# Optimization experiments

Hardware: AMD Instinct MI355X
Metric: run time of the kernel (lower is better)

The kernel has to match this reference:

```python
import jax, jax.numpy as jnp
import numpy as np

T = 5
EPS = 1e-05


def setup_inputs() -> dict:
    key = jax.random.key(0)
    X = jax.random.normal(key, (64, 512, 32, 32), dtype=jnp.float32)
    return {"X": X}


def reference(X):
    # IterNorm (training branch): whiten channels via Newton-Schulz inverse sqrt.
    N, C, H, W = X.shape
    x = jnp.transpose(X, (1, 0, 2, 3)).reshape(C, -1)  # [d, m], d=C, m=N*H*W
    d, m = x.shape
    mean = jnp.mean(x, axis=-1, keepdims=True)
    xc = x - mean
    I = jnp.eye(d, dtype=X.dtype)
    # Sigma = eps*I + (1/m) xc xc^T  (addmm(eps, I, 1/m, xc, xc^T))
    Sigma = EPS * I + (xc @ xc.T) / m
    rTr = 1.0 / jnp.trace(Sigma)          # (Sigma * I).sum().reciprocal()
    Sigma_N = Sigma * rTr
    P = I
    for _ in range(T):
        # P_{k+1} = 1.5*P_k - 0.5 * P_k^3 @ Sigma_N
        P = 1.5 * P - 0.5 * (P @ P @ P) @ Sigma_N
    wm = P * jnp.sqrt(rTr)                # whitening matrix ~ Sigma^{-1/2}
    xn = wm @ xc                          # [d, m]
    Xn = jnp.transpose(xn.reshape(C, N, H, W), (1, 0, 2, 3))
    return Xn
```

## Files before the change

### kernel.cpp

```cpp
#include <hip/hip_runtime.h>
#include <math.h>

#define Nn   64
#define Cc   512
#define HWs  1024
#define CHW  (Cc * HWs)
#define Mm   (Nn * HWs)
#define EPSC 1e-5f
#define NBC  128

typedef unsigned int   u32;
typedef unsigned short u16;
typedef unsigned long long u64;
typedef __attribute__((ext_vector_type(8))) short  short8;
typedef __attribute__((ext_vector_type(4))) float  floatx4;

__device__ __forceinline__ u16 f2bf(float f) {
    u32 u = __float_as_uint(f);
    u += 0x7fff + ((u >> 16) & 1);
    return (u16)(u >> 16);
}
__device__ __forceinline__ float bf2f(u16 h) {
    return __uint_as_float(((u32)h) << 16);
}

__device__ __forceinline__ void gld_lds16(const u16* g, u16* l) {
    __builtin_amdgcn_global_load_lds(
        (const __attribute__((address_space(1))) u32*)g,
        (__attribute__((address_space(3))) u32*)l, 16, 0, 0);
}

#define AUX_SC 0x11

__device__ __forceinline__ void gld_lds16_sc(const u16* g, u16* l) {
    __builtin_amdgcn_global_load_lds(
        (const __attribute__((address_space(1))) u32*)g,
        (__attribute__((address_space(3))) u32*)l, 16, 0, AUX_SC);
}
__device__ __forceinline__ void st8_sc(u16* p, u64 pk) {
    asm volatile("global_store_dwordx2 %0, %1, off sc0 sc1"
                 :: "v"(p), "v"(pk) : "memory");
}
__device__ __forceinline__ u64 pk4(const u16* h) {
    return (u64)h[0] | ((u64)h[1] << 16) | ((u64)h[2] << 32) | ((u64)h[3] << 48);
}

__global__ __launch_bounds__(256) void convert_transpose(const float* __restrict__ X,
                                                         u16* __restrict__ Xbf,
                                                         u16* __restrict__ Xt,
                                                         float* __restrict__ meanP) {
    const int hT = blockIdx.x;
    const int h0 = hT << 6;
    const int c0 = blockIdx.y << 6;
    const int n  = blockIdx.z;
    const int t  = threadIdx.x;
    __shared__ u16   T[64][65];
    __shared__ float red[64][17];

    const float* Xn  = X   + (size_t)n * CHW;
    u16*         Xbn = Xbf + (size_t)n * CHW;
    u16*         Xtn = Xt  + (size_t)n * CHW;

    const int cl = t >> 4;
    const int h4 = (t & 15) << 2;
#pragma unroll
    for (int i = 0; i < 4; ++i) {
        const int c = cl + (i << 4);
        float4 v = *(const float4*)&Xn[(size_t)(c0 + c) * HWs + h0 + h4];
        red[c][t & 15] = v.x + v.y + v.z + v.w;
        u16 b0 = f2bf(v.x), b1 = f2bf(v.y), b2 = f2bf(v.z), b3 = f2bf(v.w);
        *(ushort4*)&Xbn[(size_t)(c0 + c) * HWs + h0 + h4] = make_ushort4(b0, b1, b2, b3);
        T[c][h4]     = b0;
        T[c][h4 + 1] = b1;
        T[c][h4 + 2] = b2;
        T[c][h4 + 3] = b3;
    }
    __syncthreads();
    const int hl = t >> 4;
    const int c4 = (t & 15) << 2;
#pragma unroll
    for (int i = 0; i < 4; ++i) {
        const int h = hl + (i << 4);
        ushort4 pk = make_ushort4(T[c4][h], T[c4 + 1][h], T[c4 + 2][h], T[c4 + 3][h]);
        *(ushort4*)&Xtn[(size_t)(h0 + h) * Cc + c0 + c4] = pk;
    }
    if (t < 64) {
        float s = 0.f;
#pragma unroll
        for (int j = 0; j < 16; ++j) s += red[t][j];
        atomicAdd(&meanP[hT * 512 + c0 + t], s);
    }
}

__global__ __launch_bounds__(256) void gram_mfma(const u16* __restrict__ Xbf,
                                                 float* __restrict__ G) {
    static const int TI[10] = {0,0,0,0,1,1,1,2,2,3};
    static const int TJ[10] = {0,1,2,3,1,2,3,2,3,3};
    const int id = blockIdx.x;
    const int q  = id >> 3;
    const int x  = q % 10;
    const int y  = (id & 7) + ((q / 10) << 3);
    const int i0 = TI[x] << 7;
    const int j0 = TJ[x] << 7;
    const int n0 = y << 1;
    const int t  = threadIdx.x;
    const int w  = t >> 6, l = t & 63;

    __shared__ u16 As[2][4096];
    __shared__ u16 Bs[2][4096];

    floatx4 acc[4][4];
#pragma unroll
    for (int mi = 0; mi < 4; ++mi)
#pragma unroll
        for (int ni = 0; ni < 4; ++ni) acc[mi][ni] = (floatx4){0.f, 0.f, 0.f, 0.f};

    const int lr = l >> 2;
    const int lc = (l & 3) << 3;
    const int wm = w >> 1, wn = w & 1;
    const int fm = l & 15, fq = l >> 4;

    auto issue = [&](int s, int bb) {
        const u16* Xn = Xbf + (size_t)(n0 + (s >> 5)) * CHW;
        const int hw  = (s & 31) << 5;
#pragma unroll
        for (int p = 0; p < 2; ++p) {
            const int g   = w * 2 + p;
            const int row = g * 16 + lr;
            gld_lds16(Xn + (size_t)(i0 + row) * HWs + hw + lc, &As[bb][g * 512]);
            gld_lds16(Xn + (size_t)(j0 + row) * HWs + hw + lc, &Bs[bb][g * 512]);
        }
    };

    issue(0, 0);
    __syncthreads();
    for (int s = 0; s < 64; ++s) {
        if (s < 63) issue(s + 1, (s + 1) & 1);
        const int bb = s & 1;
        short8 a[4], b[4];
#pragma unroll
        for (int mi = 0; mi < 4; ++mi)
            a[mi] = *(const short8*)&As[bb][(wm * 64 + mi * 16 + fm) * 32 + fq * 8];
#pragma unroll
        for (int ni = 0; ni < 4; ++ni)
            b[ni] = *(const short8*)&Bs[bb][(wn * 64 + ni * 16 + fm) * 32 + fq * 8];
#pragma unroll
        for (int mi = 0; mi < 4; ++mi)
#pragma unroll
            for (int ni = 0; ni < 4; ++ni)
                acc[mi][ni] = __builtin_amdgcn_mfma_f32_16x16x32_bf16(
                    a[mi], b[ni], acc[mi][ni], 0, 0, 0);
        __syncthreads();
    }
#pragma unroll
    for (int mi = 0; mi < 4; ++mi)
#pragma unroll
        for (int ni = 0; ni < 4; ++ni)
#pragma unroll
            for (int r = 0; r < 4; ++r) {
                const int gi = i0 + wm * 64 + mi * 16 + fq * 4 + r;
                const int gj = j0 + wn * 64 + ni * 16 + fm;
                atomicAdd(&G[(size_t)gi * Cc + gj], acc[mi][ni][r]);
            }
}

__device__ __forceinline__ void gridbar(int* bar, int gen) {
    asm volatile("s_waitcnt vmcnt(0)" ::: "memory");
    __syncthreads();
    if (threadIdx.x == 0) {
        __hip_atomic_fetch_add(bar, 1, __ATOMIC_RELAXED, __HIP_MEMORY_SCOPE_AGENT);
        while (__hip_atomic_load(bar, __ATOMIC_RELAXED, __HIP_MEMORY_SCOPE_AGENT) < gen * NBC)
            __builtin_amdgcn_s_sleep(1);
    }
    __syncthreads();
}

template <int MR>
__device__ __forceinline__ void mm_bk64(const u16* Ah, const u16* Al,
                                        const u16* Bh, const u16* Bl,
                                        int i0, int j0,
                                        float alpha, const float* D, float beta,
                                        float* Cf, u16* Ch, u16* Cl, u16* S) {
    const int t = threadIdx.x, w = t >> 6, l = t & 63;
    const int wm = w >> 1, wn = w & 1, fm = l & 15, fq = l >> 4;
    const int lr = l >> 2, lc = (l & 3) << 3;
    constexpr int MI     = MR / 32;
    constexpr int OFF_AL = MR * 64;
    constexpr int OFF_BH = 2 * MR * 64;
    constexpr int OFF_BL = 2 * MR * 64 + 4096;
    constexpr int BUFSZ  = 2 * MR * 64 + 8192;

    const u16* src  = (w == 0) ? Ah : (w == 1) ? Al : (w == 2) ? Bh : Bl;
    const int rbase = (w < 2) ? i0 : j0;
    const int R     = (w < 2) ? MR : 64;
    const int OFF   = (w == 0) ? 0 : (w == 1) ? OFF_AL : (w == 2) ? OFF_BH : OFF_BL;

    floatx4 acc[MI][2];
#pragma unroll
    for (int mi = 0; mi < MI; ++mi)
#pragma unroll
        for (int ni = 0; ni < 2; ++ni) acc[mi][ni] = (floatx4){0.f, 0.f, 0.f, 0.f};

    auto issue = [&](int c, int bb) {
        u16* dst = S + bb * BUFSZ + OFF;
        const u16* sp = src + (size_t)rbase * 512 + (c << 6);
#pragma unroll
        for (int s = 0; s < 2; ++s)
#pragma unroll 4
            for (int g = 0; g < (R >> 4); ++g)
                gld_lds16_sc(sp + (size_t)(g * 16 + lr) * 512 + s * 32 + lc,
                             dst + s * R * 32 + g * 512);
    };
    auto compute = [&](int bb) {
        const u16* base = S + bb * BUFSZ;
#pragma unroll
        for (int s = 0; s < 2; ++s) {
            short8 ah[MI], al[MI], bh[2], bl[2];
#pragma unroll
            for (int mi = 0; mi < MI; ++mi) {
                const int r = wm * (MR / 2) + mi * 16 + fm;
                const int o = s * MR * 32 + r * 32 + fq * 8;
                ah[mi] = *(const short8*)&base[o];
                al[mi] = *(const short8*)&base[OFF_AL + o];
            }
#pragma unroll
            for (int ni = 0; ni < 2; ++ni) {
                const int r = wn * 32 + ni * 16 + fm;
                const int o = s * 2048 + r * 32 + fq * 8;
                bh[ni] = *(const short8*)&base[OFF_BH + o];
                bl[ni] = *(const short8*)&base[OFF_BL + o];
            }
#pragma unroll
            for (int mi = 0; mi < MI; ++mi)
#pragma unroll
                for (int ni = 0; ni < 2; ++ni) {
                    acc[mi][ni] = __builtin_amdgcn_mfma_f32_16x16x32_bf16(ah[mi], bh[ni], acc[mi][ni], 0, 0, 0);
                    acc[mi][ni] = __builtin_amdgcn_mfma_f32_16x16x32_bf16(ah[mi], bl[ni], acc[mi][ni], 0, 0, 0);
                    acc[mi][ni] = __builtin_amdgcn_mfma_f32_16x16x32_bf16(al[mi], bh[ni], acc[mi][ni], 0, 0, 0);
                }
        }
    };

    issue(0, 0);
    __syncthreads();
    for (int c = 0; c < 8; ++c) {
        if (c < 7) issue(c + 1, (c + 1) & 1);
        compute(c & 1);
        __syncthreads();
    }

#pragma unroll
    for (int mi = 0; mi < MI; ++mi)
#pragma unroll
        for (int ni = 0; ni < 2; ++ni) {
            const int gib = i0 + wm * (MR / 2) + mi * 16 + fq * 4;
            const int gj  = j0 + wn * 32 + ni * 16 + fm;
            u16 h[4], lo[4];
#pragma unroll
            for (int r4 = 0; r4 < 4; ++r4) {
                float v = alpha * acc[mi][ni][r4];
                if (D) v += beta * D[(size_t)(gib + r4) * 512 + gj];
                if (Cf) Cf[(size_t)(gib + r4) * 512 + gj] = v;
                h[r4]  = f2bf(v);
                lo[r4] = f2bf(v - bf2f(h[r4]));
            }
            st8_sc(&Ch[(size_t)gj * 512 + gib], pk4(h));
            st8_sc(&Cl[(size_t)gj * 512 + gib], pk4(lo));
        }
}

__global__ __launch_bounds__(256) void ns_chain(
    const float* G, const float* meanP, float* scal, int* bar, float* wmmv,
    u16* Sh, u16* Sl, u16* PhA, u16* PlA, u16* PhB, u16* PlB,
    u16* T2h, u16* T2l, u16* Wh, u16* Wl, float* PfA, float* PfB) {
    __shared__ u16   S[32768];
    __shared__ float meanL[512];
    __shared__ float redL[4];
    const int t = threadIdx.x, b = blockIdx.x;
    const int w = t >> 6, l = t & 63;

    float tp = 0.f;
#pragma unroll
    for (int cb = 0; cb < 2; ++cb) {
        const int c = t + (cb << 8);
        float s = 0.f;
#pragma unroll
        for (int q = 0; q < 16; ++q) s += meanP[(q << 9) + c];
        const float mc = s * (1.0f / Mm);
        meanL[c] = mc;
        tp += G[(size_t)c * 513] * (1.0f / Mm) - mc * mc;
    }
#pragma unroll
    for (int o = 32; o > 0; o >>= 1) tp += __shfl_xor(tp, o);
    if (l == 0) redL[w] = tp;
    __syncthreads();
    const float tr  = redL[0] + redL[1] + redL[2] + redL[3] + (float)Cc * EPSC;
    const float rtr = 1.0f / tr;
    const float sr  = sqrtf(rtr);
    if (b == 0 && t == 0) { scal[0] = rtr; scal[1] = sr; }

    const int R0 = (b >> 3) << 5;
    const int C0 = (b & 7) << 6;
#pragma unroll
    for (int k2 = 0; k2 < 2; ++k2) {
        const int idx4 = (k2 << 8) + t;
        const int i  = R0 + (idx4 >> 4);
        const int jb = C0 + ((idx4 & 15) << 2);
        float p1[4];
        u16 sh[4], sl[4], ph[4], pl[4];
#pragma unroll
        for (int u = 0; u < 4; ++u) {
            const int j = jb + u;
            const float g = (i <= j) ? G[((size_t)i << 9) + j] : G[((size_t)j << 9) + i];
            float sig = g * (1.0f / Mm) - meanL[i] * meanL[j];
            if (i == j) sig += EPSC;
            const float sN = sig * rtr;
            sh[u] = f2bf(sN);
            sl[u] = f2bf(sN - bf2f(sh[u]));
            p1[u] = ((i == j) ? 1.5f : 0.f) - 0.5f * sN;
            ph[u] = f2bf(p1[u]);
            pl[u] = f2bf(p1[u] - bf2f(ph[u]));
        }
        const size_t e = ((size_t)i << 9) + jb;
        st8_sc(&Sh[e],  pk4(sh));
        st8_sc(&Sl[e],  pk4(sl));
        st8_sc(&PhA[e], pk4(ph));
        st8_sc(&PlA[e], pk4(pl));
        *(float4*)&PfA[e] = make_float4(p1[0], p1[1], p1[2], p1[3]);
    }
    int gen = 0;
    gridbar(bar, ++gen);

    u16 *ph = PhA, *pl = PlA, *qh = PhB, *ql = PlB;
    float *pf = PfA, *qf = PfB;
    const int i0a = ((b & 63) >> 3) << 6, j0a = (b & 7) << 6;
    for (int it = 0; it < 4; ++it) {
        if (b < 64)
            mm_bk64<64>(ph, pl, ph, pl, i0a, j0a, 1.f, nullptr, 0.f,
                        nullptr, T2h, T2l, S);
        else
            mm_bk64<64>(ph, pl, Sh, Sl, i0a, j0a, 1.f, nullptr, 0.f,
                        nullptr, Wh, Wl, S);
        gridbar(bar, ++gen);
        mm_bk64<32>(T2h, T2l, Wh, Wl, R0, C0, -0.5f, pf, 1.5f,
                    qf, qh, ql, S);
        gridbar(bar, ++gen);
        { u16* x = ph; ph = qh; qh = x; }
        { u16* x = pl; pl = ql; ql = x; }
        { float* x = pf; pf = qf; qf = x; }
    }

    {
        const int row = R0 + (t >> 3);
        const int jb  = C0 + ((t & 7) << 3);
        float s = 0.f;
#pragma unroll
        for (int jj = 0; jj < 8; ++jj)
            s += pf[((size_t)row << 9) + jb + jj] * meanL[jb + jj];
        s += __shfl_xor(s, 1);
        s += __shfl_xor(s, 2);
        s += __shfl_xor(s, 4);
        if ((t & 7) == 0) atomicAdd(&wmmv[row], s * sr);
    }
}

__global__ __launch_bounds__(256) void whiten_mfma(const u16* __restrict__ Xt,
                                                   const u16* __restrict__ Pbf,
                                                   const float* __restrict__ wmm,
                                                   const float* __restrict__ scal,
                                                   float* __restrict__ out) {
    const int id  = blockIdx.x;
    const int m   = (id >> 3) & 3;
    const int grp = (id & 7) + ((id >> 5) << 3);
    const int c0  = m << 7;
    const int h0  = (grp & 3) << 8;
    const int n   = grp >> 2;
    const int t   = threadIdx.x;
    const int w   = t >> 6, l = t & 63;

    __shared__ char smem[49152];
    u16* As = (u16*)smem;
    u16* Bs = As + 16384;
    float* Ep = (float*)smem;

    floatx4 acc[8][4];
#pragma unroll
    for (int mi = 0; mi < 8; ++mi)
#pragma unroll
        for (int ni = 0; ni < 4; ++ni) acc[mi][ni] = (floatx4){0.f, 0.f, 0.f, 0.f};

    const int lr = l >> 2;
    const int lc = (l & 3) << 3;
    const int wm = w >> 1, wn = w & 1;
    const int fm = l & 15, fq = l >> 4;

    const u16* Xn = Xt + (size_t)n * CHW;

    auto issue = [&](int k, int bb) {
        const int kk = k << 5;
#pragma unroll
        for (int gi = 0; gi < 4; ++gi) {
            const int g = w * 4 + gi;
            gld_lds16(Xn + (size_t)(h0 + g * 16 + lr) * Cc + kk + lc,
                      &As[bb * 8192 + g * 512]);
        }
#pragma unroll
        for (int p = 0; p < 2; ++p) {
            const int g = w * 2 + p;
            gld_lds16(Pbf + (size_t)(c0 + g * 16 + lr) * Cc + kk + lc,
                      &Bs[bb * 4096 + g * 512]);
        }
    };

    issue(0, 0);
    __syncthreads();
    for (int k = 0; k < 16; ++k) {
        if (k < 15) issue(k + 1, (k + 1) & 1);
        const int bb = k & 1;
        short8 a[8], b[4];
#pragma unroll
        for (int mi = 0; mi < 8; ++mi)
            a[mi] = *(const short8*)&As[bb * 8192 + (wm * 128 + mi * 16 + fm) * 32 + fq * 8];
#pragma unroll
        for (int ni = 0; ni < 4; ++ni)
            b[ni] = *(const short8*)&Bs[bb * 4096 + (wn * 64 + ni * 16 + fm) * 32 + fq * 8];
#pragma unroll
        for (int mi = 0; mi < 8; ++mi)
#pragma unroll
            for (int ni = 0; ni < 4; ++ni)
                acc[mi][ni] = __builtin_amdgcn_mfma_f32_16x16x32_bf16(
                    a[mi], b[ni], acc[mi][ni], 0, 0, 0);
        __syncthreads();
    }

    const float sr = scal[1];
    float wv[4];
#pragma unroll
    for (int ni = 0; ni < 4; ++ni) wv[ni] = wmm[c0 + wn * 64 + ni * 16 + fm];
    float* outn = out + (size_t)n * CHW;

#pragma unroll
    for (int mp = 0; mp < 4; ++mp) {
        __syncthreads();
#pragma unroll
        for (int p = 0; p < 2; ++p) {
            const int mi = mp * 2 + p;
#pragma unroll
            for (int ni = 0; ni < 4; ++ni) {
                const int row  = wn * 64 + ni * 16 + fm;
                const int slot = wm * 32 + p * 16 + fq * 4;
                floatx4 v = acc[mi][ni] * sr - wv[ni];
                *(floatx4*)&Ep[row * 68 + slot] = v;
            }
        }
        __syncthreads();
#pragma unroll
        for (int jj = 0; jj < 8; ++jj) {
            const int idx = jj * 256 + t;
            const int row = idx >> 4;
            const int s4  = (idx & 15) << 2;
            const int wmr = s4 >> 5;
            const int within = s4 & 31;
            float4 v = *(const float4*)&Ep[row * 68 + s4];
            *(float4*)&outn[(size_t)(c0 + row) * HWs + h0 + wmr * 128 + mp * 32 + within] = v;
        }
    }
}

__global__ __launch_bounds__(256) void mean_kernel(const float* __restrict__ X,
                                                   float* __restrict__ mean) {
    const int c = blockIdx.x;
    const int t = threadIdx.x;
    float s = 0.f;
    for (int n = 0; n < Nn; ++n) {
        const float4* p = (const float4*)(X + (size_t)n * CHW + (size_t)c * HWs);
        float4 v = p[t];
        s += v.x + v.y + v.z + v.w;
    }
    __shared__ float red[256];
    red[t] = s;
    __syncthreads();
    for (int o = 128; o > 0; o >>= 1) {
        if (t < o) red[t] += red[t + o];
        __syncthreads();
    }
    if (t == 0) mean[c] = red[0] * (1.0f / Mm);
}

__global__ __launch_bounds__(256) void trace_fb(const float* __restrict__ G,
                                                const float* __restrict__ mean,
                                                float* __restrict__ scal) {
    const int t = threadIdx.x;
    float s = 0.f;
    for (int i = t; i < Cc; i += 256)
        s += G[(size_t)i * Cc + i] * (1.0f / Mm) - mean[i] * mean[i];
    __shared__ float red[256];
    red[t] = s;
    __syncthreads();
    for (int o = 128; o > 0; o >>= 1) {
        if (t < o) red[t] += red[t + o];
        __syncthreads();
    }
    if (t == 0) {
        const float tr  = red[0] + (float)Cc * EPSC;
        const float rtr = 1.0f / tr;
        scal[0] = rtr;
        scal[1] = sqrtf(rtr);
    }
}

__global__ __launch_bounds__(256) void gram_kernel(const float* __restrict__ X,
                                                   float* __restrict__ G) {
    const int ti = blockIdx.x >> 3, tj = blockIdx.x & 7;
    const int i0 = ti << 6, j0 = tj << 6;
    const int n0 = blockIdx.y << 3;
    const int t  = threadIdx.x;
    const int tx = t & 15, ty = t >> 4;
    __shared__ float As[64][33];
    __shared__ float Bs[64][33];
    float acc[4][4] = {};
    const int lc = t & 31;
    const int lr0 = t >> 5;
    for (int n = n0; n < n0 + 8; ++n) {
        const float* Xn = X + (size_t)n * CHW;
        for (int hw0 = 0; hw0 < HWs; hw0 += 32) {
#pragma unroll
            for (int r = 0; r < 8; ++r) {
                const int row = lr0 + (r << 3);
                As[row][lc] = Xn[(size_t)(i0 + row) * HWs + hw0 + lc];
                Bs[row][lc] = Xn[(size_t)(j0 + row) * HWs + hw0 + lc];
            }
            __syncthreads();
#pragma unroll
            for (int k = 0; k < 32; ++k) {
                float a[4], b[4];
#pragma unroll
                for (int r = 0; r < 4; ++r) a[r] = As[(ty << 2) + r][k];
#pragma unroll
                for (int cn = 0; cn < 4; ++cn) b[cn] = Bs[(tx << 2) + cn][k];
#pragma unroll
                for (int r = 0; r < 4; ++r)
#pragma unroll
                    for (int cn = 0; cn < 4; ++cn) acc[r][cn] += a[r] * b[cn];
            }
            __syncthreads();
        }
    }
#pragma unroll
    for (int r = 0; r < 4; ++r)
#pragma unroll
        for (int cn = 0; cn < 4; ++cn)
            atomicAdd(&G[(size_t)(i0 + (ty << 2) + r) * Cc + j0 + (tx << 2) + cn],
                      acc[r][cn]);
}

__global__ __launch_bounds__(256) void sigman_full_kernel(const float* __restrict__ G,
                                                          const float* __restrict__ mean,
                                                          const float* __restrict__ scal,
                                                          float* __restrict__ S,
                                                          float* __restrict__ P) {
    const int e = blockIdx.x * 256 + threadIdx.x;
    const int i = e >> 9, j = e & 511;
    const float rtr = scal[0];
    float sig = G[e] * (1.0f / Mm) - mean[i] * mean[j];
    if (i == j) sig += EPSC;
    S[e] = sig * rtr;
    P[e] = (i == j) ? 1.f : 0.f;
}

__global__ __launch_bounds__(256) void mm512_kernel(const float* __restrict__ A,
                                                    const float* __restrict__ B,
                                                    float* __restrict__ C,
                                                    float alpha,
                                                    const float* __restrict__ D,
                                                    float beta) {
    const int ti = blockIdx.x >> 3, tj = blockIdx.x & 7;
    const int i0 = ti << 6, j0 = tj << 6;
    const int t  = threadIdx.x;
    const int tx = t & 15, ty = t >> 4;
    __shared__ float As[64][33];
    __shared__ float Bs[32][65];
    float acc[4][4] = {};
    const int lcA = t & 31, lrA = t >> 5;
    const int lcB = t & 63, lrB = t >> 6;
    for (int k0 = 0; k0 < 512; k0 += 32) {
#pragma unroll
        for (int r = 0; r < 8; ++r) {
            const int row = lrA + (r << 3);
            As[row][lcA] = A[(size_t)(i0 + row) * 512 + k0 + lcA];
        }
#pragma unroll
        for (int r = 0; r < 8; ++r) {
            const int row = lrB + (r << 2);
            Bs[row][lcB] = B[(size_t)(k0 + row) * 512 + j0 + lcB];
        }
        __syncthreads();
#pragma unroll
        for (int k = 0; k < 32; ++k) {
            float a[4], b[4];
#pragma unroll
            for (int r = 0; r < 4; ++r) a[r] = As[(ty << 2) + r][k];
#pragma unroll
            for (int cn = 0; cn < 4; ++cn) b[cn] = Bs[k][(tx << 2) + cn];
#pragma unroll
            for (int r = 0; r < 4; ++r)
#pragma unroll
                for (int cn = 0; cn < 4; ++cn) acc[r][cn] += a[r] * b[cn];
        }
        __syncthreads();
    }
#pragma unroll
    for (int r = 0; r < 4; ++r) {
        const size_t idx = (size_t)(i0 + (ty << 2) + r) * 512 + j0 + (tx << 2);
        float4 v;
        v.x = alpha * acc[r][0];
        v.y = alpha * acc[r][1];
        v.z = alpha * acc[r][2];
        v.w = alpha * acc[r][3];
        if (D) {
            const float4 d = *(const float4*)(D + idx);
            v.x += beta * d.x; v.y += beta * d.y; v.z += beta * d.z; v.w += beta * d.w;
        }
        *(float4*)(C + idx) = v;
    }
}

__global__ __launch_bounds__(128) void wmm_kernel(const float* __restrict__ P,
                                                  const float* __restrict__ mean,
                                                  const float* __restrict__ scal,
                                                  float* __restrict__ wmm) {
    const int c = blockIdx.x, t = threadIdx.x;
    float s = 0.f;
    for (int j = t; j < Cc; j += 128) s += P[(size_t)c * Cc + j] * mean[j];
    __shared__ float red[128];
    red[t] = s;
    __syncthreads();
    for (int o = 64; o > 0; o >>= 1) {
        if (t < o) red[t] += red[t + o];
        __syncthreads();
    }
    if (t == 0) wmm[c] = red[0] * scal[1];
}

__global__ __launch_bounds__(256) void whiten_kernel(const float* __restrict__ X,
                                                     const float* __restrict__ P,
                                                     const float* __restrict__ wmm,
                                                     const float* __restrict__ scal,
                                                     float* __restrict__ out) {
    const int c0 = blockIdx.x << 6;
    const int h0 = blockIdx.y << 6;
    const int n  = blockIdx.z;
    const int t  = threadIdx.x;
    const int tx = t & 15, ty = t >> 4;
    __shared__ float Ps[64][33];
    __shared__ float Xs[32][65];
    float acc[4][4] = {};
    const int lcA = t & 31, lrA = t >> 5;
    const int lcB = t & 63, lrB = t >> 6;
    const float* Xn = X + (size_t)n * CHW;
    for (int k0 = 0; k0 < 512; k0 += 32) {
#pragma unroll
        for (int r = 0; r < 8; ++r) {
            const int row = lrA + (r << 3);
            Ps[row][lcA] = P[(size_t)(c0 + row) * 512 + k0 + lcA];
        }
#pragma unroll
        for (int r = 0; r < 8; ++r) {
            const int row = lrB + (r << 2);
            Xs[row][lcB] = Xn[(size_t)(k0 + row) * HWs + h0 + lcB];
        }
        __syncthreads();
#pragma unroll
        for (int k = 0; k < 32; ++k) {
            float a[4], b[4];
#pragma unroll
            for (int r = 0; r < 4; ++r) a[r] = Ps[(ty << 2) + r][k];
#pragma unroll
            for (int cn = 0; cn < 4; ++cn) b[cn] = Xs[k][(tx << 2) + cn];
#pragma unroll
            for (int r = 0; r < 4; ++r)
#pragma unroll
                for (int cn = 0; cn < 4; ++cn) acc[r][cn] += a[r] * b[cn];
        }
        __syncthreads();
    }
    const float sr = scal[1];
#pragma unroll
    for (int r = 0; r < 4; ++r) {
        const int c = c0 + (ty << 2) + r;
        const float wv = wmm[c];
        float4 v;
        v.x = sr * acc[r][0] - wv;
        v.y = sr * acc[r][1] - wv;
        v.z = sr * acc[r][2] - wv;
        v.w = sr * acc[r][3] - wv;
        *(float4*)(out + (size_t)n * CHW + (size_t)c * HWs + h0 + (tx << 2)) = v;
    }
}

extern "C" void kernel_launch(void* const* d_in, const int* in_sizes, int n_in,
                              void* d_out, int out_size, void* d_ws, size_t ws_size,
                              hipStream_t stream) {
    const float* X = (const float*)d_in[0];
    float* out     = (float*)d_out;

    const size_t NU16 = 33554432;
    const size_t NM   = 262144;
    const size_t NEED = NU16 * 2 * 2
                      + NM * 10 * 2
                      + (NM + 8192 + 32 + 512 + 512 + 2 * NM) * 4;

    if (ws_size >= NEED) {
        u16* Xbf = (u16*)d_ws;
        u16* Xt  = Xbf + NU16;
        u16* Sh  = Xt  + NU16;
        u16* Sl  = Sh + NM;
        u16* PhA = Sl + NM;
        u16* PlA = PhA + NM;
        u16* PhB = PlA + NM;
        u16* PlB = PhB + NM;
        u16* T2h = PlB + NM;
        u16* T2l = T2h + NM;
        u16* Wh  = T2l + NM;
        u16* Wl  = Wh + NM;
        float* G     = (float*)(Wl + NM);
        float* meanP = G + NM;
        float* scal  = meanP + 8192;
        int*   bar   = (int*)(scal + 16);
        float* mean  = (float*)(bar + 16);
        float* wmm   = mean + 512;
        float* PfA   = wmm + 512;
        float* PfB   = PfA + NM;

        hipMemsetAsync(G, 0, (NM + 8192 + 32 + 1024) * sizeof(float), stream);
        convert_transpose<<<dim3(16, 8, 64), 256, 0, stream>>>(X, Xbf, Xt, meanP);
        gram_mfma<<<320, 256, 0, stream>>>(Xbf, G);
        ns_chain<<<NBC, 256, 0, stream>>>(G, meanP, scal, bar, wmm,
                                          Sh, Sl, PhA, PlA, PhB, PlB,
                                          T2h, T2l, Wh, Wl, PfA, PfB);
        whiten_mfma<<<1024, 256, 0, stream>>>(Xt, PhA, wmm, scal, out);
    } else {
        float* ws   = (float*)d_ws;
        float* mean = ws;
        float* wmm  = ws + 512;
        float* scal = ws + 1024;
        float* G    = ws + 2048;
        float* S    = G + 262144;
        float* Pa   = S + 262144;
        float* Pb   = Pa + 262144;
        float* P2   = Pb + 262144;
        float* P3   = P2 + 262144;

        mean_kernel<<<512, 256, 0, stream>>>(X, mean);
        hipMemsetAsync(G, 0, sizeof(float) * 262144, stream);
        gram_kernel<<<dim3(64, 8), 256, 0, stream>>>(X, G);
        trace_fb<<<1, 256, 0, stream>>>(G, mean, scal);
        sigman_full_kernel<<<1024, 256, 0, stream>>>(G, mean, scal, S, Pa);

        float* P  = Pa;
        float* Pn = Pb;
        for (int it = 0; it < 5; ++it) {
            mm512_kernel<<<64, 256, 0, stream>>>(P, P, P2, 1.f, nullptr, 0.f);
            mm512_kernel<<<64, 256, 0, stream>>>(P2, P, P3, 1.f, nullptr, 0.f);
            mm512_kernel<<<64, 256, 0, stream>>>(P3, S, Pn, -0.5f, P, 1.5f);
            float* tmp = P; P = Pn; Pn = tmp;
        }

        wmm_kernel<<<512, 128, 0, stream>>>(P, mean, scal, wmm);
        whiten_kernel<<<dim3(8, 16, 64), 256, 0, stream>>>(X, P, wmm, scal, out);
    }
}
```

Before: 464.7 us.

## Prefetch two stages ahead with partial vmcnt waits and raw barriers in GEMM loops

Restructures the double-buffered LDS loading in three GEMM kernels: two tiles are issued before the loop, and each iteration waits only for the older tile's loads using s_waitcnt vmcnt(N) with the count set by how many loads each wave issued. It then synchronises with a bare s_barrier, and the next-but-one tile is issued into the freed buffer after compute. This keeps more global->LDS loads in flight and avoids the full vmcnt(0) drain that __syncthreads implies. The risk is correctness if the vmcnt counts do not match the per-wave load counts, or if the compiler inserts other memory ops between them.

```diff
diff --git a/kernel.cpp b/kernel.cpp
--- a/kernel.cpp
+++ b/kernel.cpp
@@ -44,6 +44,9 @@
 __device__ __forceinline__ u64 pk4(const u16* h) {
     return (u64)h[0] | ((u64)h[1] << 16) | ((u64)h[2] << 32) | ((u64)h[3] << 48);
 }
+
+#define WAITV(N) asm volatile("s_waitcnt vmcnt(" #N ")" ::: "memory")
+#define RAWBAR() __builtin_amdgcn_s_barrier()
 
 __global__ __launch_bounds__(256) void convert_transpose(const float* __restrict__ X,
                                                          u16* __restrict__ Xbf,
@@ -133,9 +136,10 @@
     };
 
     issue(0, 0);
-    __syncthreads();
+    issue(1, 1);
     for (int s = 0; s < 64; ++s) {
-        if (s < 63) issue(s + 1, (s + 1) & 1);
+        if (s < 63) WAITV(4); else WAITV(0);
+        RAWBAR();
         const int bb = s & 1;
         short8 a[4], b[4];
 #pragma unroll
@@ -150,7 +154,8 @@
             for (int ni = 0; ni < 4; ++ni)
                 acc[mi][ni] = __builtin_amdgcn_mfma_f32_16x16x32_bf16(
                     a[mi], b[ni], acc[mi][ni], 0, 0, 0);
-        __syncthreads();
+        RAWBAR();
+        if (s < 62) issue(s + 2, bb);
     }
 #pragma unroll
     for (int mi = 0; mi < 4; ++mi)
@@ -211,6 +216,11 @@
                 gld_lds16_sc(sp + (size_t)(g * 16 + lr) * 512 + s * 32 + lc,
                              dst + s * R * 32 + g * 512);
     };
+    auto waitL = [&](bool last) {
+        if (last) { WAITV(0); return; }
+        if (MR == 64) { WAITV(8); }
+        else if (w < 2) { WAITV(4); } else { WAITV(8); }
+    };
     auto compute = [&](int bb) {
         const u16* base = S + bb * BUFSZ;
 #pragma unroll
@@ -242,11 +252,13 @@
     };
 
     issue(0, 0);
-    __syncthreads();
+    issue(1, 1);
     for (int c = 0; c < 8; ++c) {
-        if (c < 7) issue(c + 1, (c + 1) & 1);
+        waitL(c == 7);
+        RAWBAR();
         compute(c & 1);
-        __syncthreads();
+        RAWBAR();
+        if (c < 6) issue(c + 2, c & 1);
     }
 
 #pragma unroll
@@ -413,9 +425,10 @@
     };
 
     issue(0, 0);
-    __syncthreads();
+    issue(1, 1);
     for (int k = 0; k < 16; ++k) {
-        if (k < 15) issue(k + 1, (k + 1) & 1);
+        if (k < 15) WAITV(6); else WAITV(0);
+        RAWBAR();
         const int bb = k & 1;
         short8 a[8], b[4];
 #pragma unroll
@@ -430,7 +443,8 @@
             for (int ni = 0; ni < 4; ++ni)
                 acc[mi][ni] = __builtin_amdgcn_mfma_f32_16x16x32_bf16(
                     a[mi], b[ni], acc[mi][ni], 0, 0, 0);
-        __syncthreads();
+        RAWBAR();
+        if (k < 14) issue(k + 2, bb);
     }
 
     const float sr = scal[1];
```

New measurement: 458.7 us. No clear change (-1.3%).
